# Kernel optimization log

Hardware: AMD Instinct MI355X
Metric: run time of the kernel (lower is better)

The kernel has to match this reference:

```python
import jax, jax.numpy as jnp
import numpy as np

S, B, E = 2048, 2, 1024
H = 16
HD = E // H
RANK = 8
ALPHA = 16.0
LORA_SCALE = ALPHA / RANK


def setup_inputs() -> dict:
    key = jax.random.key(0)
    ks = jax.random.split(key, 13)
    d = {
        'query': jax.random.normal(ks[0], (S, B, E), jnp.float32),
        'key': jax.random.normal(ks[1], (S, B, E), jnp.float32),
        'value': jax.random.normal(ks[2], (S, B, E), jnp.float32),
        'in_proj_weight': jax.random.normal(ks[3], (3 * E, E), jnp.float32) * 0.02,
        'in_proj_bias': jax.random.normal(ks[4], (3 * E,), jnp.float32) * 0.02,
        'out_w': jax.random.normal(ks[5], (E, E), jnp.float32) * 0.02,
        'out_b': jax.random.normal(ks[6], (E,), jnp.float32) * 0.02,
        'A_q': jax.random.normal(ks[7], (RANK, E), jnp.float32) * 0.02,
        'B_q': jax.random.normal(ks[8], (E, RANK), jnp.float32) * 0.02,
        'A_k': jax.random.normal(ks[9], (RANK, E), jnp.float32) * 0.02,
        'B_k': jax.random.normal(ks[10], (E, RANK), jnp.float32) * 0.02,
        'A_v': jax.random.normal(ks[11], (RANK, E), jnp.float32) * 0.02,
        'B_v': jax.random.normal(ks[12], (E, RANK), jnp.float32) * 0.02,
    }
    return d


def _proj(x, W, b, A, Bm):
    # frozen linear + LoRA low-rank delta: x @ W.T + b + ((x @ A.T) @ B.T) * scale
    base = jnp.einsum('sbe,fe->sbf', x, W) + b
    lora = jnp.einsum('sbr,fr->sbf', jnp.einsum('sbe,re->sbr', x, A), Bm) * LORA_SCALE
    return base + lora


def reference(query, key, value, in_proj_weight, in_proj_bias, out_w, out_b,
              A_q, B_q, A_k, B_k, A_v, B_v):
    Wq, Wk, Wv = in_proj_weight[:E], in_proj_weight[E:2 * E], in_proj_weight[2 * E:]
    bq, bk, bv = in_proj_bias[:E], in_proj_bias[E:2 * E], in_proj_bias[2 * E:]
    q = _proj(query, Wq, bq, A_q, B_q)   # [S,B,E]
    k = _proj(key, Wk, bk, A_k, B_k)
    v = _proj(value, Wv, bv, A_v, B_v)
    # reshape to [B*H, S, HD] (seq-first layout, matching torch view/transpose)
    def heads(x):
        return x.reshape(S, B * H, HD).transpose(1, 0, 2)
    qh, kh, vh = heads(q), heads(k), heads(v)
    scale = HD ** -0.5
    attn = jnp.einsum('nsd,ntd->nst', qh, kh) * scale  # [B*H,S,S]
    attn = jax.nn.softmax(attn, axis=-1)
    out = jnp.einsum('nst,ntd->nsd', attn, vh)         # [B*H,S,HD]
    out = out.transpose(1, 0, 2).reshape(S, B, E)
    out = jnp.einsum('sbe,fe->sbf', out, out_w) + out_b
    return out
```

## Files before the change

### kernel.cpp

```cpp
#include <hip/hip_runtime.h>
#include <stdint.h>

static const int S_ = 2048, B_ = 2, E_ = 1024, H_ = 16, HD_ = 64, MR_ = 4096;

typedef __bf16 bf16;
typedef __bf16 bf16x8 __attribute__((ext_vector_type(8)));
typedef float  f32x4  __attribute__((ext_vector_type(4)));
typedef float  f32x16 __attribute__((ext_vector_type(16)));
typedef unsigned short u16x8 __attribute__((ext_vector_type(8)));

#define AS1(p) ((const __attribute__((address_space(1))) void*)(p))
#define AS3(p) ((__attribute__((address_space(3))) void*)(p))

#define QSCALE 0.18033688011112042f

static __device__ __forceinline__ uint32_t cvtpk_bf16(float lo, float hi) {
    uint32_t r;
    asm("v_cvt_pk_bf16_f32 %0, %1, %2" : "=v"(r) : "v"(lo), "v"(hi));
    return r;
}

__global__ __launch_bounds__(256) void cvt_all(const float* __restrict__ s0,
                                               const float* __restrict__ s1,
                                               const float* __restrict__ s2,
                                               const float* __restrict__ s3,
                                               bf16* __restrict__ d0,
                                               bf16* __restrict__ d1,
                                               bf16* __restrict__ d2,
                                               bf16* __restrict__ d3) {
    int b = blockIdx.x;
    const float* src;
    bf16* dst;
    int i;
    if (b < 6144) {
        int seg = b >> 11;
        i = (b & 2047) * 256 + threadIdx.x;
        src = seg == 0 ? s0 : (seg == 1 ? s1 : s2);
        dst = seg == 0 ? d0 : (seg == 1 ? d1 : d2);
    } else {
        i = (b - 6144) * 256 + threadIdx.x;
        src = s3; dst = d3;
    }
    const float4* s = (const float4*)src;
    float4 a = s[i * 2], c = s[i * 2 + 1];
    bf16x8 v;
    v[0] = (bf16)a.x; v[1] = (bf16)a.y; v[2] = (bf16)a.z; v[3] = (bf16)a.w;
    v[4] = (bf16)c.x; v[5] = (bf16)c.y; v[6] = (bf16)c.z; v[7] = (bf16)c.w;
    *(bf16x8*)(dst + (size_t)i * 8) = v;
}

__global__ __launch_bounds__(256) void build_weff3(const float* __restrict__ W,
                                                   const float* __restrict__ A0,
                                                   const float* __restrict__ B0,
                                                   const float* __restrict__ A1,
                                                   const float* __restrict__ B1,
                                                   const float* __restrict__ A2,
                                                   const float* __restrict__ B2,
                                                   bf16* __restrict__ o0,
                                                   bf16* __restrict__ o1,
                                                   bf16* __restrict__ o2) {
    int z = blockIdx.y;
    const float* A = z == 0 ? A0 : (z == 1 ? A1 : A2);
    const float* Bm = z == 0 ? B0 : (z == 1 ? B1 : B2);
    bf16* out = z == 0 ? o0 : (z == 1 ? o1 : o2);
    const float* Wz = W + (size_t)z * 1024 * 1024;
    int idx = blockIdx.x * 256 + threadIdx.x;
    int f = idx >> 10, e = idx & 1023;
    float acc = Wz[idx];
#pragma unroll
    for (int r = 0; r < 8; r++) acc += 2.0f * Bm[f * 8 + r] * A[r * 1024 + e];
    out[idx] = (bf16)acc;
}

__global__ __launch_bounds__(256) void gemm_qkv(const bf16* __restrict__ XQ,
                                                const bf16* __restrict__ XK,
                                                const bf16* __restrict__ XV,
                                                const bf16* __restrict__ WQ,
                                                const bf16* __restrict__ WK,
                                                const bf16* __restrict__ WV,
                                                const float* __restrict__ ipb,
                                                bf16* __restrict__ QH,
                                                bf16* __restrict__ KH,
                                                bf16* __restrict__ VH) {
    int z = blockIdx.z;
    const bf16* Amat = z == 0 ? XQ : (z == 1 ? XK : XV);
    const bf16* Bmat = z == 0 ? WQ : (z == 1 ? WK : WV);
    bf16* Cout = z == 0 ? QH : (z == 1 ? KH : VH);
    const float* bias = ipb + z * 1024;
    float cscale = z == 0 ? QSCALE : 1.0f;

    __shared__ bf16 smbuf[16896];
    const int tid = threadIdx.x;
    const int wid = tid >> 6, lane = tid & 63;
    const int lg = lane >> 4, li = lane & 15;
    const int bidl = blockIdx.y * 8 + blockIdx.x;
    const int orig = (bidl & 7) * 32 + (bidl >> 3);
    const int m0 = (orig >> 3) * 128, n0 = (orig & 7) * 128;
    const int wr = wid >> 1, wc = wid & 1;

    f32x4 acc[4][4] = {};

    for (int kt = 0; kt < 1024; kt += 64) {
        __syncthreads();
#pragma unroll
        for (int h = 0; h < 2; h++)
#pragma unroll
            for (int i = 0; i < 2; i++) {
                int c = wid * 2 + i;
                const bf16* ga = Amat + (size_t)(m0 + c * 16 + (lane >> 2)) * 1024 + kt + h * 32 + (lane & 3) * 8;
                __builtin_amdgcn_global_load_lds(AS1(ga), AS3(smbuf + h * 4096 + c * 512), 16, 0, 0);
                const bf16* gb = Bmat + (size_t)(n0 + c * 16 + (lane >> 2)) * 1024 + kt + h * 32 + (lane & 3) * 8;
                __builtin_amdgcn_global_load_lds(AS1(gb), AS3(smbuf + 8192 + h * 4096 + c * 512), 16, 0, 0);
            }
        __syncthreads();

#pragma unroll
        for (int h = 0; h < 2; h++) {
            bf16x8 a[4], b[4];
#pragma unroll
            for (int mi = 0; mi < 4; mi++)
                a[mi] = *(const bf16x8*)(smbuf + h * 4096 + (wr * 64 + mi * 16 + li) * 32 + lg * 8);
#pragma unroll
            for (int ni = 0; ni < 4; ni++)
                b[ni] = *(const bf16x8*)(smbuf + 8192 + h * 4096 + (wc * 64 + ni * 16 + li) * 32 + lg * 8);
#pragma unroll
            for (int mi = 0; mi < 4; mi++)
#pragma unroll
                for (int ni = 0; ni < 4; ni++)
                    acc[mi][ni] = __builtin_amdgcn_mfma_f32_16x16x32_bf16(a[mi], b[ni], acc[mi][ni], 0, 0, 0);
        }
    }

    __syncthreads();
#pragma unroll
    for (int ni = 0; ni < 4; ni++) {
        int fl = wc * 64 + ni * 16 + li;
        float bv = bias[n0 + fl];
#pragma unroll
        for (int mi = 0; mi < 4; mi++)
#pragma unroll
            for (int r = 0; r < 4; r++) {
                int ml_ = wr * 64 + mi * 16 + lg * 4 + r;
                smbuf[ml_ * 132 + fl] = (bf16)((acc[mi][ni][r] + bv) * cscale);
            }
    }
    __syncthreads();
#pragma unroll
    for (int k = 0; k < 8; k++) {
        int c = tid + 256 * k;
        int dhalf = c & 7, m = (c >> 3) & 127, hl = c >> 10;
        u16x8 v = *(const u16x8*)(smbuf + m * 132 + hl * 64 + dhalf * 8);
        int mg = m0 + m, fg = n0 + hl * 64;
        int s = mg >> 1, bb = mg & 1, h = fg >> 6, d = dhalf * 8;
        *(u16x8*)(Cout + (size_t)(bb * 16 + h) * S_ * 64 + (size_t)s * 64 + d) = v;
    }
}

__global__ __launch_bounds__(256) void gemm_out64(const bf16* __restrict__ Amat,
                                                  const bf16* __restrict__ Bmat,
                                                  const float* __restrict__ bias,
                                                  float* __restrict__ Cout) {
    __shared__ bf16 Asm[2][64 * 32];
    __shared__ bf16 Bsm[2][128 * 32];
    const int tid = threadIdx.x;
    const int wid = tid >> 6, lane = tid & 63;
    const int lg = lane >> 4, li = lane & 15;
    const int bidl = blockIdx.y * 8 + blockIdx.x;
    const int orig = (bidl & 7) * 64 + (bidl >> 3);
    const int m0 = (orig >> 3) * 64, n0 = (orig & 7) * 128;
    const int wr = wid >> 1, wc = wid & 1;

    f32x4 acc[2][4] = {};

    for (int kt = 0; kt < 1024; kt += 64) {
        __syncthreads();
#pragma unroll
        for (int h = 0; h < 2; h++)
            for (int j = wid; j < 12; j += 4) {
                if (j < 4) {
                    const bf16* ga = Amat + (size_t)(m0 + j * 16 + (lane >> 2)) * 1024 + kt + h * 32 + (lane & 3) * 8;
                    __builtin_amdgcn_global_load_lds(AS1(ga), AS3(&Asm[h][j * 512]), 16, 0, 0);
                } else {
                    int c = j - 4;
                    const bf16* gb = Bmat + (size_t)(n0 + c * 16 + (lane >> 2)) * 1024 + kt + h * 32 + (lane & 3) * 8;
                    __builtin_amdgcn_global_load_lds(AS1(gb), AS3(&Bsm[h][c * 512]), 16, 0, 0);
                }
            }
        __syncthreads();

#pragma unroll
        for (int h = 0; h < 2; h++) {
            bf16x8 a[2], b[4];
#pragma unroll
            for (int mi = 0; mi < 2; mi++)
                a[mi] = *(const bf16x8*)(&Asm[h][(wr * 32 + mi * 16 + li) * 32 + lg * 8]);
#pragma unroll
            for (int ni = 0; ni < 4; ni++)
                b[ni] = *(const bf16x8*)(&Bsm[h][(wc * 64 + ni * 16 + li) * 32 + lg * 8]);
#pragma unroll
            for (int mi = 0; mi < 2; mi++)
#pragma unroll
                for (int ni = 0; ni < 4; ni++)
                    acc[mi][ni] = __builtin_amdgcn_mfma_f32_16x16x32_bf16(a[mi], b[ni], acc[mi][ni], 0, 0, 0);
        }
    }

#pragma unroll
    for (int ni = 0; ni < 4; ni++) {
        int f = n0 + wc * 64 + ni * 16 + li;
        float bv = bias[f];
#pragma unroll
        for (int mi = 0; mi < 2; mi++)
#pragma unroll
            for (int r = 0; r < 4; r++) {
                int m = m0 + wr * 32 + mi * 16 + lg * 4 + r;
                Cout[(size_t)m * 1024 + f] = acc[mi][ni][r] + bv;
            }
    }
}

__global__ __launch_bounds__(256, 4) void attn_fwd(const bf16* __restrict__ qh,
                                                   const bf16* __restrict__ kh,
                                                   const bf16* __restrict__ vh,
                                                   bf16* __restrict__ outbuf) {
    __shared__ __attribute__((aligned(16))) char smem[33280];

    const int bid = blockIdx.x;
    const int head = (bid & 7) * 4 + ((bid >> 3) & 3);
    const int qt = bid >> 5;
    const int tid = threadIdx.x, wid = tid >> 6, l = tid & 63;
    const int li = l & 31, hi = l >> 5;
    const int kvh = wid & 1;

    const bf16* Qb = qh + (size_t)head * S_ * 64;
    const bf16* Kb = kh + (size_t)head * S_ * 64;
    const bf16* Vb = vh + (size_t)head * S_ * 64;
    const int q0 = qt * 64 + (wid >> 1) * 32;

    bf16x8 qf[4];
#pragma unroll
    for (int s = 0; s < 4; s++)
        qf[s] = *(const bf16x8*)(Qb + (size_t)(q0 + li) * 64 + 16 * s + 8 * hi);

    f32x16 oacc0 = {}, oacc1 = {};
    float lsum = 0.f;

    const size_t kg_off = ((size_t)(16 * (l & 7)) ^ (16 * ((l >> 3) & 7)));
    const int vk2 = tid & 31, vdb = (tid >> 5) * 8;
    const int rswz = 16 * (li & 7);

#define STAGE_K(kv0, dstbuf)                                                    \
    {                                                                           \
        _Pragma("unroll")                                                       \
        for (int j = 0; j < 2; j++) {                                           \
            int row = (j * 4 + wid) * 8 + (l >> 3);                             \
            const char* srcp = (const char*)Kb + (size_t)((kv0) + row) * 128 + kg_off; \
            __builtin_amdgcn_global_load_lds(AS1(srcp),                         \
                AS3((dstbuf) + (j * 4 + wid) * 1024), 16, 0, 0);                \
        }                                                                       \
    }

    u16x8 vreg0, vreg1;
    vreg0 = *(const u16x8*)(Vb + (size_t)(2 * vk2) * 64 + vdb);
    vreg1 = *(const u16x8*)(Vb + (size_t)(2 * vk2 + 1) * 64 + vdb);
    STAGE_K(0, smem);

    for (int t = 0; t < 32; t++) {
        const int cur = t & 1;
        char* Kc = smem + cur * 8192;
        char* Vc = smem + 16384 + cur * 8192;
#pragma unroll
        for (int i = 0; i < 8; i++) {
            uint32_t w = (uint32_t)vreg0[i] | ((uint32_t)vreg1[i] << 16);
            *(uint32_t*)(Vc + (vdb + i) * 128 + ((4 * vk2) ^ (16 * i))) = w;
        }
        __syncthreads();
        if (t + 1 < 32) {
            int kv0 = (t + 1) * 64;
            vreg0 = *(const u16x8*)(Vb + (size_t)(kv0 + 2 * vk2) * 64 + vdb);
            vreg1 = *(const u16x8*)(Vb + (size_t)(kv0 + 2 * vk2 + 1) * 64 + vdb);
            STAGE_K(kv0, smem + (cur ^ 1) * 8192);
        }

        f32x16 s = {};
        __builtin_amdgcn_s_setprio(1);
#pragma unroll
        for (int step = 0; step < 4; step++) {
            bf16x8 k0 = *(const bf16x8*)(Kc + (kvh * 32 + li) * 128 + ((32 * step + 16 * hi) ^ rswz));
            s = __builtin_amdgcn_mfma_f32_32x32x16_bf16(k0, qf[step], s, 0, 0, 0);
        }
        __builtin_amdgcn_s_setprio(0);

        float p[16];
#pragma unroll
        for (int r = 0; r < 16; r++) p[r] = __builtin_amdgcn_exp2f(s[r]);
        lsum += (((p[0] + p[1]) + (p[2] + p[3])) + ((p[4] + p[5]) + (p[6] + p[7]))) +
                (((p[8] + p[9]) + (p[10] + p[11])) + ((p[12] + p[13]) + (p[14] + p[15])));

        bf16x8 pa[2];
#pragma unroll
        for (int st = 0; st < 2; st++) {
            uint32_t a0 = cvtpk_bf16(p[8 * st + 0], p[8 * st + 1]);
            uint32_t a1 = cvtpk_bf16(p[8 * st + 2], p[8 * st + 3]);
            uint32_t b0 = cvtpk_bf16(p[8 * st + 4], p[8 * st + 5]);
            uint32_t b1 = cvtpk_bf16(p[8 * st + 6], p[8 * st + 7]);
            asm("v_permlane32_swap_b32 %0, %1" : "+v"(a0), "+v"(b0));
            asm("v_permlane32_swap_b32 %0, %1" : "+v"(a1), "+v"(b1));
            union { uint32_t u[4]; bf16x8 v; } pu;
            pu.u[0] = a0; pu.u[1] = a1; pu.u[2] = b0; pu.u[3] = b1;
            pa[st] = pu.v;
        }

        __builtin_amdgcn_s_setprio(1);
#pragma unroll
        for (int st = 0; st < 2; st++) {
            int byteoff = (64 * kvh + 32 * st + 16 * hi) ^ rswz;
            bf16x8 v0 = *(const bf16x8*)(Vc + li * 128 + byteoff);
            oacc0 = __builtin_amdgcn_mfma_f32_32x32x16_bf16(pa[st], v0, oacc0, 0, 0, 0);
            bf16x8 v1 = *(const bf16x8*)(Vc + (32 + li) * 128 + byteoff);
            oacc1 = __builtin_amdgcn_mfma_f32_32x32x16_bf16(pa[st], v1, oacc1, 0, 0, 0);
        }
        __builtin_amdgcn_s_setprio(0);
    }

    __syncthreads();
    float* mlp = (float*)(smem + 32768);
    float* scr = (float*)smem;
    float lt = lsum + __shfl_xor(lsum, 32);
    if (l < 32) mlp[wid * 32 + l] = lt;
    {
        float* mys = scr + wid * 1024;
#pragma unroll
        for (int r = 0; r < 16; r++) {
            int rp = (r & 3) + 8 * (r >> 2) + 4 * hi;
            mys[rp * 32 + li] = kvh ? oacc0[r] : oacc1[r];
        }
    }
    __syncthreads();
    float pl = mlp[(wid ^ 1) * 32 + li];
    float linv = 1.0f / (lt + pl);
    const float* ps = scr + (wid ^ 1) * 1024;
    int bb = head >> 4, h = head & 15;
#pragma unroll
    for (int r = 0; r < 16; r++) {
        int rp = (r & 3) + 8 * (r >> 2) + 4 * hi;
        int q = q0 + rp;
        float own = kvh ? oacc1[r] : oacc0[r];
        float part = ps[rp * 32 + li];
        float val = (own + part) * __shfl(linv, rp);
        outbuf[(size_t)(q * 2 + bb) * 1024 + h * 64 + kvh * 32 + li] = (bf16)val;
    }
}

extern "C" void kernel_launch(void* const* d_in, const int* in_sizes, int n_in,
                              void* d_out, int out_size, void* d_ws, size_t ws_size,
                              hipStream_t stream) {
    const float* query = (const float*)d_in[0];
    const float* key_  = (const float*)d_in[1];
    const float* value = (const float*)d_in[2];
    const float* ipw   = (const float*)d_in[3];
    const float* ipb   = (const float*)d_in[4];
    const float* out_w = (const float*)d_in[5];
    const float* out_b = (const float*)d_in[6];
    const float* A_q   = (const float*)d_in[7];
    const float* B_q   = (const float*)d_in[8];
    const float* A_k   = (const float*)d_in[9];
    const float* B_k   = (const float*)d_in[10];
    const float* A_v   = (const float*)d_in[11];
    const float* B_v   = (const float*)d_in[12];

    const size_t MB = 1ull << 20;
    if (ws_size < 64 * MB) return;
    char* ws = (char*)d_ws;
    bf16* XQ = (bf16*)(ws + 0 * MB);
    bf16* XK = (bf16*)(ws + 8 * MB);
    bf16* XV = (bf16*)(ws + 16 * MB);
    bf16* WQ = (bf16*)(ws + 24 * MB);
    bf16* WK = (bf16*)(ws + 26 * MB);
    bf16* WV = (bf16*)(ws + 28 * MB);
    bf16* WO = (bf16*)(ws + 30 * MB);
    bf16* QH = (bf16*)(ws + 32 * MB);
    bf16* KH = (bf16*)(ws + 40 * MB);
    bf16* VH = (bf16*)(ws + 48 * MB);
    bf16* AT = (bf16*)(ws + 56 * MB);

    cvt_all<<<6656, 256, 0, stream>>>(query, key_, value, out_w, XQ, XK, XV, WO);
    build_weff3<<<dim3(4096, 3), 256, 0, stream>>>(ipw, A_q, B_q, A_k, B_k, A_v, B_v,
                                                   WQ, WK, WV);

    gemm_qkv<<<dim3(8, 32, 3), 256, 0, stream>>>(XQ, XK, XV, WQ, WK, WV, ipb, QH, KH, VH);

    attn_fwd<<<1024, 256, 0, stream>>>(QH, KH, VH, AT);

    gemm_out64<<<dim3(8, 64), 256, 0, stream>>>(AT, WO, out_b, (float*)d_out);
}
```

Before: 129.1 us.

## Load K fragments directly into registers, drop K LDS staging, reswizzle V

The attention kernel no longer stages K tiles through LDS with global_load_lds. Each lane reads its own K row fragments from global memory into registers and prefetches the next tile during softmax. The V LDS layout switches to an 8-byte-granularity swizzle read with split 64-bit loads, and the main loop is unrolled by two. Halving LDS use could raise occupancy and removes the K LDS traffic, but K is now read redundantly from global/L2 by both wave pairs, and register pressure goes up.

```diff
diff --git a/kernel.cpp b/kernel.cpp
--- a/kernel.cpp
+++ b/kernel.cpp
@@ -223,7 +223,7 @@
                                                    const bf16* __restrict__ kh,
                                                    const bf16* __restrict__ vh,
                                                    bf16* __restrict__ outbuf) {
-    __shared__ __attribute__((aligned(16))) char smem[33280];
+    __shared__ __attribute__((aligned(16))) char smem[16896];
 
     const int bid = blockIdx.x;
     const int head = (bid & 7) * 4 + ((bid >> 3) & 3);
@@ -242,54 +242,50 @@
     for (int s = 0; s < 4; s++)
         qf[s] = *(const bf16x8*)(Qb + (size_t)(q0 + li) * 64 + 16 * s + 8 * hi);
 
+    const bf16* Krow = Kb + (size_t)(kvh * 32 + li) * 64 + 8 * hi;
+
     f32x16 oacc0 = {}, oacc1 = {};
     float lsum = 0.f;
 
-    const size_t kg_off = ((size_t)(16 * (l & 7)) ^ (16 * ((l >> 3) & 7)));
     const int vk2 = tid & 31, vdb = (tid >> 5) * 8;
-    const int rswz = 16 * (li & 7);
-
-#define STAGE_K(kv0, dstbuf)                                                    \
-    {                                                                           \
-        _Pragma("unroll")                                                       \
-        for (int j = 0; j < 2; j++) {                                           \
-            int row = (j * 4 + wid) * 8 + (l >> 3);                             \
-            const char* srcp = (const char*)Kb + (size_t)((kv0) + row) * 128 + kg_off; \
-            __builtin_amdgcn_global_load_lds(AS1(srcp),                         \
-                AS3((dstbuf) + (j * 4 + wid) * 1024), 16, 0, 0);                \
-        }                                                                       \
-    }
+    const int vswz = 8 * (li & 15);
 
     u16x8 vreg0, vreg1;
     vreg0 = *(const u16x8*)(Vb + (size_t)(2 * vk2) * 64 + vdb);
     vreg1 = *(const u16x8*)(Vb + (size_t)(2 * vk2 + 1) * 64 + vdb);
-    STAGE_K(0, smem);
-
+    bf16x8 kf[4], kn[4];
+#pragma unroll
+    for (int st = 0; st < 4; st++)
+        kf[st] = *(const bf16x8*)(Krow + 16 * st);
+
+#pragma unroll 2
     for (int t = 0; t < 32; t++) {
         const int cur = t & 1;
-        char* Kc = smem + cur * 8192;
-        char* Vc = smem + 16384 + cur * 8192;
+        char* Vc = smem + cur * 8192;
 #pragma unroll
         for (int i = 0; i < 8; i++) {
             uint32_t w = (uint32_t)vreg0[i] | ((uint32_t)vreg1[i] << 16);
-            *(uint32_t*)(Vc + (vdb + i) * 128 + ((4 * vk2) ^ (16 * i))) = w;
+            *(uint32_t*)(Vc + (vdb + i) * 128 + ((4 * vk2) ^ (8 * ((vdb + i) & 15)))) = w;
         }
         __syncthreads();
         if (t + 1 < 32) {
             int kv0 = (t + 1) * 64;
             vreg0 = *(const u16x8*)(Vb + (size_t)(kv0 + 2 * vk2) * 64 + vdb);
             vreg1 = *(const u16x8*)(Vb + (size_t)(kv0 + 2 * vk2 + 1) * 64 + vdb);
-            STAGE_K(kv0, smem + (cur ^ 1) * 8192);
         }
 
         f32x16 s = {};
         __builtin_amdgcn_s_setprio(1);
 #pragma unroll
-        for (int step = 0; step < 4; step++) {
-            bf16x8 k0 = *(const bf16x8*)(Kc + (kvh * 32 + li) * 128 + ((32 * step + 16 * hi) ^ rswz));
-            s = __builtin_amdgcn_mfma_f32_32x32x16_bf16(k0, qf[step], s, 0, 0, 0);
-        }
+        for (int step = 0; step < 4; step++)
+            s = __builtin_amdgcn_mfma_f32_32x32x16_bf16(kf[step], qf[step], s, 0, 0, 0);
         __builtin_amdgcn_s_setprio(0);
+
+        if (t + 1 < 32) {
+#pragma unroll
+            for (int st = 0; st < 4; st++)
+                kn[st] = *(const bf16x8*)(Krow + (size_t)(t + 1) * 4096 + 16 * st);
+        }
 
         float p[16];
 #pragma unroll
@@ -314,17 +310,27 @@
         __builtin_amdgcn_s_setprio(1);
 #pragma unroll
         for (int st = 0; st < 2; st++) {
-            int byteoff = (64 * kvh + 32 * st + 16 * hi) ^ rswz;
-            bf16x8 v0 = *(const bf16x8*)(Vc + li * 128 + byteoff);
-            oacc0 = __builtin_amdgcn_mfma_f32_32x32x16_bf16(pa[st], v0, oacc0, 0, 0, 0);
-            bf16x8 v1 = *(const bf16x8*)(Vc + (32 + li) * 128 + byteoff);
-            oacc1 = __builtin_amdgcn_mfma_f32_32x32x16_bf16(pa[st], v1, oacc1, 0, 0, 0);
+            int p0 = (64 * kvh + 32 * st + 16 * hi) ^ vswz;
+            const char* r0 = Vc + li * 128;
+            const char* r1 = Vc + (32 + li) * 128;
+            union { uint64_t d[2]; bf16x8 v; } u0, u1;
+            u0.d[0] = *(const uint64_t*)(r0 + p0);
+            u0.d[1] = *(const uint64_t*)(r0 + (p0 ^ 8));
+            u1.d[0] = *(const uint64_t*)(r1 + p0);
+            u1.d[1] = *(const uint64_t*)(r1 + (p0 ^ 8));
+            oacc0 = __builtin_amdgcn_mfma_f32_32x32x16_bf16(pa[st], u0.v, oacc0, 0, 0, 0);
+            oacc1 = __builtin_amdgcn_mfma_f32_32x32x16_bf16(pa[st], u1.v, oacc1, 0, 0, 0);
         }
         __builtin_amdgcn_s_setprio(0);
+
+        if (t + 1 < 32) {
+#pragma unroll
+            for (int st = 0; st < 4; st++) kf[st] = kn[st];
+        }
     }
 
     __syncthreads();
-    float* mlp = (float*)(smem + 32768);
+    float* mlp = (float*)(smem + 16384);
     float* scr = (float*)smem;
     float lt = lsum + __shfl_xor(lsum, 32);
     if (l < 32) mlp[wid * 32 + l] = lt;
```

After: 237.4 us. 83.9% more time.

## Double-buffer GEMM LDS staging and reswizzle V tile in attention

Applied to the files above, without the earlier changes.

The QKV and output-projection GEMMs now use two LDS buffers of 32-wide K slices. The next slice is prefetched with global_load_lds while the current one feeds MFMAs, so each iteration needs one barrier instead of two. In attention, the V tile's LDS write swizzle changes to an 8-byte XOR pattern keyed on row, and each V fragment is read as two 64-bit loads to cut bank conflicts. The cost is more LDS instructions per V fragment and a single-barrier scheme that depends on the async loads having landed in time.

```diff
diff --git a/kernel.cpp b/kernel.cpp
--- a/kernel.cpp
+++ b/kernel.cpp
@@ -100,35 +100,41 @@
 
     f32x4 acc[4][4] = {};
 
-    for (int kt = 0; kt < 1024; kt += 64) {
+#define QKV_STAGE(t)                                                            \
+    {                                                                           \
+        int bsel = (t) & 1;                                                     \
+        _Pragma("unroll")                                                       \
+        for (int i = 0; i < 2; i++) {                                           \
+            int c = wid * 2 + i;                                                \
+            const bf16* ga = Amat + (size_t)(m0 + c * 16 + (lane >> 2)) * 1024  \
+                             + (t) * 32 + (lane & 3) * 8;                       \
+            __builtin_amdgcn_global_load_lds(AS1(ga),                           \
+                AS3(smbuf + bsel * 8192 + c * 512), 16, 0, 0);                  \
+            const bf16* gb = Bmat + (size_t)(n0 + c * 16 + (lane >> 2)) * 1024  \
+                             + (t) * 32 + (lane & 3) * 8;                       \
+            __builtin_amdgcn_global_load_lds(AS1(gb),                           \
+                AS3(smbuf + bsel * 8192 + 4096 + c * 512), 16, 0, 0);           \
+        }                                                                       \
+    }
+
+    QKV_STAGE(0);
+    for (int t = 0; t < 32; t++) {
         __syncthreads();
-#pragma unroll
-        for (int h = 0; h < 2; h++)
-#pragma unroll
-            for (int i = 0; i < 2; i++) {
-                int c = wid * 2 + i;
-                const bf16* ga = Amat + (size_t)(m0 + c * 16 + (lane >> 2)) * 1024 + kt + h * 32 + (lane & 3) * 8;
-                __builtin_amdgcn_global_load_lds(AS1(ga), AS3(smbuf + h * 4096 + c * 512), 16, 0, 0);
-                const bf16* gb = Bmat + (size_t)(n0 + c * 16 + (lane >> 2)) * 1024 + kt + h * 32 + (lane & 3) * 8;
-                __builtin_amdgcn_global_load_lds(AS1(gb), AS3(smbuf + 8192 + h * 4096 + c * 512), 16, 0, 0);
-            }
-        __syncthreads();
-
-#pragma unroll
-        for (int h = 0; h < 2; h++) {
-            bf16x8 a[4], b[4];
-#pragma unroll
-            for (int mi = 0; mi < 4; mi++)
-                a[mi] = *(const bf16x8*)(smbuf + h * 4096 + (wr * 64 + mi * 16 + li) * 32 + lg * 8);
+        if (t + 1 < 32) QKV_STAGE(t + 1);
+        const bf16* Ab = smbuf + (t & 1) * 8192;
+        const bf16* Bb = Ab + 4096;
+        bf16x8 a[4], b[4];
+#pragma unroll
+        for (int mi = 0; mi < 4; mi++)
+            a[mi] = *(const bf16x8*)(Ab + (wr * 64 + mi * 16 + li) * 32 + lg * 8);
+#pragma unroll
+        for (int ni = 0; ni < 4; ni++)
+            b[ni] = *(const bf16x8*)(Bb + (wc * 64 + ni * 16 + li) * 32 + lg * 8);
+#pragma unroll
+        for (int mi = 0; mi < 4; mi++)
 #pragma unroll
             for (int ni = 0; ni < 4; ni++)
-                b[ni] = *(const bf16x8*)(smbuf + 8192 + h * 4096 + (wc * 64 + ni * 16 + li) * 32 + lg * 8);
-#pragma unroll
-            for (int mi = 0; mi < 4; mi++)
-#pragma unroll
-                for (int ni = 0; ni < 4; ni++)
-                    acc[mi][ni] = __builtin_amdgcn_mfma_f32_16x16x32_bf16(a[mi], b[ni], acc[mi][ni], 0, 0, 0);
-        }
+                acc[mi][ni] = __builtin_amdgcn_mfma_f32_16x16x32_bf16(a[mi], b[ni], acc[mi][ni], 0, 0, 0);
     }
 
     __syncthreads();
@@ -160,8 +166,7 @@
                                                   const bf16* __restrict__ Bmat,
                                                   const float* __restrict__ bias,
                                                   float* __restrict__ Cout) {
-    __shared__ bf16 Asm[2][64 * 32];
-    __shared__ bf16 Bsm[2][128 * 32];
+    __shared__ bf16 smbuf[12288];
     const int tid = threadIdx.x;
     const int wid = tid >> 6, lane = tid & 63;
     const int lg = lane >> 4, li = lane & 15;
@@ -172,37 +177,43 @@
 
     f32x4 acc[2][4] = {};
 
-    for (int kt = 0; kt < 1024; kt += 64) {
+#define OUT_STAGE(t)                                                            \
+    {                                                                           \
+        int bsel = (t) & 1;                                                     \
+        for (int j = wid; j < 12; j += 4) {                                     \
+            if (j < 4) {                                                        \
+                const bf16* ga = Amat + (size_t)(m0 + j * 16 + (lane >> 2)) * 1024 \
+                                 + (t) * 32 + (lane & 3) * 8;                   \
+                __builtin_amdgcn_global_load_lds(AS1(ga),                       \
+                    AS3(smbuf + bsel * 6144 + j * 512), 16, 0, 0);              \
+            } else {                                                            \
+                int c = j - 4;                                                  \
+                const bf16* gb = Bmat + (size_t)(n0 + c * 16 + (lane >> 2)) * 1024 \
+                                 + (t) * 32 + (lane & 3) * 8;                   \
+                __builtin_amdgcn_global_load_lds(AS1(gb),                       \
+                    AS3(smbuf + bsel * 6144 + 2048 + c * 512), 16, 0, 0);       \
+            }                                                                   \
+        }                                                                       \
+    }
+
+    OUT_STAGE(0);
+    for (int t = 0; t < 32; t++) {
         __syncthreads();
-#pragma unroll
-        for (int h = 0; h < 2; h++)
-            for (int j = wid; j < 12; j += 4) {
-                if (j < 4) {
-                    const bf16* ga = Amat + (size_t)(m0 + j * 16 + (lane >> 2)) * 1024 + kt + h * 32 + (lane & 3) * 8;
-                    __builtin_amdgcn_global_load_lds(AS1(ga), AS3(&Asm[h][j * 512]), 16, 0, 0);
-                } else {
-                    int c = j - 4;
-                    const bf16* gb = Bmat + (size_t)(n0 + c * 16 + (lane >> 2)) * 1024 + kt + h * 32 + (lane & 3) * 8;
-                    __builtin_amdgcn_global_load_lds(AS1(gb), AS3(&Bsm[h][c * 512]), 16, 0, 0);
-                }
-            }
-        __syncthreads();
-
-#pragma unroll
-        for (int h = 0; h < 2; h++) {
-            bf16x8 a[2], b[4];
-#pragma unroll
-            for (int mi = 0; mi < 2; mi++)
-                a[mi] = *(const bf16x8*)(&Asm[h][(wr * 32 + mi * 16 + li) * 32 + lg * 8]);
+        if (t + 1 < 32) OUT_STAGE(t + 1);
+        const bf16* Ab = smbuf + (t & 1) * 6144;
+        const bf16* Bb = Ab + 2048;
+        bf16x8 a[2], b[4];
+#pragma unroll
+        for (int mi = 0; mi < 2; mi++)
+            a[mi] = *(const bf16x8*)(Ab + (wr * 32 + mi * 16 + li) * 32 + lg * 8);
+#pragma unroll
+        for (int ni = 0; ni < 4; ni++)
+            b[ni] = *(const bf16x8*)(Bb + (wc * 64 + ni * 16 + li) * 32 + lg * 8);
+#pragma unroll
+        for (int mi = 0; mi < 2; mi++)
 #pragma unroll
             for (int ni = 0; ni < 4; ni++)
-                b[ni] = *(const bf16x8*)(&Bsm[h][(wc * 64 + ni * 16 + li) * 32 + lg * 8]);
-#pragma unroll
-            for (int mi = 0; mi < 2; mi++)
-#pragma unroll
-                for (int ni = 0; ni < 4; ni++)
-                    acc[mi][ni] = __builtin_amdgcn_mfma_f32_16x16x32_bf16(a[mi], b[ni], acc[mi][ni], 0, 0, 0);
-        }
+                acc[mi][ni] = __builtin_amdgcn_mfma_f32_16x16x32_bf16(a[mi], b[ni], acc[mi][ni], 0, 0, 0);
     }
 
 #pragma unroll
@@ -248,6 +259,7 @@
     const size_t kg_off = ((size_t)(16 * (l & 7)) ^ (16 * ((l >> 3) & 7)));
     const int vk2 = tid & 31, vdb = (tid >> 5) * 8;
     const int rswz = 16 * (li & 7);
+    const int vswz = 8 * (li & 15);
 
 #define STAGE_K(kv0, dstbuf)                                                    \
     {                                                                           \
@@ -272,7 +284,7 @@
 #pragma unroll
         for (int i = 0; i < 8; i++) {
             uint32_t w = (uint32_t)vreg0[i] | ((uint32_t)vreg1[i] << 16);
-            *(uint32_t*)(Vc + (vdb + i) * 128 + ((4 * vk2) ^ (16 * i))) = w;
+            *(uint32_t*)(Vc + (vdb + i) * 128 + ((4 * vk2) ^ (8 * ((vdb + i) & 15)))) = w;
         }
         __syncthreads();
         if (t + 1 < 32) {
@@ -314,11 +326,16 @@
         __builtin_amdgcn_s_setprio(1);
 #pragma unroll
         for (int st = 0; st < 2; st++) {
-            int byteoff = (64 * kvh + 32 * st + 16 * hi) ^ rswz;
-            bf16x8 v0 = *(const bf16x8*)(Vc + li * 128 + byteoff);
-            oacc0 = __builtin_amdgcn_mfma_f32_32x32x16_bf16(pa[st], v0, oacc0, 0, 0, 0);
-            bf16x8 v1 = *(const bf16x8*)(Vc + (32 + li) * 128 + byteoff);
-            oacc1 = __builtin_amdgcn_mfma_f32_32x32x16_bf16(pa[st], v1, oacc1, 0, 0, 0);
+            int p0 = (64 * kvh + 32 * st + 16 * hi) ^ vswz;
+            const char* r0 = Vc + li * 128;
+            const char* r1 = Vc + (32 + li) * 128;
+            union { uint64_t d[2]; bf16x8 v; } u0, u1;
+            u0.d[0] = *(const uint64_t*)(r0 + p0);
+            u0.d[1] = *(const uint64_t*)(r0 + (p0 ^ 8));
+            u1.d[0] = *(const uint64_t*)(r1 + p0);
+            u1.d[1] = *(const uint64_t*)(r1 + (p0 ^ 8));
+            oacc0 = __builtin_amdgcn_mfma_f32_32x32x16_bf16(pa[st], u0.v, oacc0, 0, 0, 0);
+            oacc1 = __builtin_amdgcn_mfma_f32_32x32x16_bf16(pa[st], u1.v, oacc1, 0, 0, 0);
         }
         __builtin_amdgcn_s_setprio(0);
     }
```

New measurement: 134.2 us. 4.0% more time.
